# Performance work log

Measured on AMD Instinct MI355X. Metric: run time of the kernel, lower is better.

Reference implementation:

```python
import jax, jax.numpy as jnp
import numpy as np

# dims: d_model=96, d_expand=192, d_state N=16, dt_rank R=6, K=4 scans, 3x3 depthwise conv
B_, H_, W_, DM = 2, 64, 64, 96
DEXP, N, R, K, DCONV = 192, 16, 6, 4, 3


def setup_inputs() -> dict:
    key = jax.random.key(0)
    ks = jax.random.split(key, 8)
    s = lambda k, shape, scale: jax.random.normal(k, shape, jnp.float32) * scale
    return {
        "x": jax.random.normal(ks[0], (B_, H_, W_, DM), jnp.float32),
        "in_proj_w": s(ks[1], (2 * DEXP, DM), 0.05),          # Linear(d_model -> 2*d_expand), no bias
        "conv_w": s(ks[2], (DEXP, 1, DCONV, DCONV), 0.1),     # depthwise conv2d
        "conv_b": jnp.zeros((DEXP,), jnp.float32),
        "x_proj_weight": s(ks[3], (K, R + 2 * N, DEXP), 0.05),
        "dt_projs_weight": s(ks[4], (K, DEXP, R), 0.1),
        "dt_projs_bias": s(ks[5], (K, DEXP), 0.1),
        "A_logs": jnp.tile(jnp.log(jnp.arange(1, N + 1, dtype=jnp.float32))[None, :], (K * DEXP, 1)),
        "Ds": jnp.ones((K * DEXP,), jnp.float32),
        "out_norm_scale": jnp.ones((DEXP,), jnp.float32),
        "out_norm_bias": jnp.zeros((DEXP,), jnp.float32),
        "out_proj_w": s(ks[6], (DM, DEXP), 0.05),             # Linear(d_expand -> d_model), no bias
    }


def _selective_scan(u, delta, A, Bmat, Cmat, Ds):
    # u, delta: (B,K,D,L); A: (K,D,N); Bmat, Cmat: (B,K,N,L); Ds: (K,D)
    Bb, Kk, Dd, L = u.shape
    u_t = jnp.moveaxis(u, -1, 0)      # (L,B,K,D)
    d_t = jnp.moveaxis(delta, -1, 0)  # (L,B,K,D)
    B_t = jnp.moveaxis(Bmat, -1, 0)   # (L,B,K,N)
    C_t = jnp.moveaxis(Cmat, -1, 0)   # (L,B,K,N)
    h0 = jnp.zeros((Bb, Kk, Dd, A.shape[-1]), u.dtype)

    def step(h, inp):
        dt, ut, bt, ct = inp
        dA = jnp.exp(dt[..., None] * A)                      # (B,K,D,N)
        h = dA * h + (dt * ut)[..., None] * bt[:, :, None, :]
        y = jnp.einsum('bkdn,bkn->bkd', h, ct)
        return h, y

    _, ys = jax.lax.scan(step, h0, (d_t, u_t, B_t, C_t))
    ys = jnp.moveaxis(ys, 0, -1)                             # (B,K,D,L)
    return ys + u * Ds[None, :, :, None]


def reference(x, in_proj_w, conv_w, conv_b, x_proj_weight, dt_projs_weight,
              dt_projs_bias, A_logs, Ds, out_norm_scale, out_norm_bias, out_proj_w):
    B, H, W, _ = x.shape
    L = H * W
    # in_proj then split into ssm branch and gate
    xz = x @ in_proj_w.T                                     # (B,H,W,2*DEXP)
    xp, z = jnp.split(xz, 2, axis=-1)
    z = jax.nn.silu(z)
    # depthwise conv (NCHW) + SiLU
    xc = jnp.transpose(xp, (0, 3, 1, 2))                     # (B,DEXP,H,W)
    xc = jax.lax.conv_general_dilated(
        xc, conv_w, (1, 1), [(1, 1), (1, 1)],
        dimension_numbers=('NCHW', 'OIHW', 'NCHW'),
        feature_group_count=DEXP) + conv_b[None, :, None, None]
    xc = jax.nn.silu(xc)
    # multi-directional scan: h, h_flip, v, v_flip  (v = flatten in (w h) order)
    xh = xc.reshape(B, DEXP, L)
    xv = jnp.transpose(xc, (0, 1, 3, 2)).reshape(B, DEXP, L)
    xs = jnp.stack([xh, xh[..., ::-1], xv, xv[..., ::-1]], axis=1)  # (B,K,D,L)
    # per-direction projections
    x_dbl = jnp.einsum('bkdl,kcd->bkcl', xs, x_proj_weight)
    dts, Bs, Cs = jnp.split(x_dbl, [R, R + N], axis=2)
    dts = jnp.einsum('bkrl,kdr->bkdl', dts, dt_projs_weight)
    delta = jax.nn.softplus(dts + dt_projs_bias[None, :, :, None])
    A = -jnp.exp(A_logs).reshape(K, DEXP, N)
    ys = _selective_scan(xs, delta, A, Bs, Cs, Ds.reshape(K, DEXP))  # (B,K,D,L)
    # merge: reverse each scan back to row-major order, then sum
    yh = ys[:, 0]
    yhf = ys[:, 1][..., ::-1]
    yv = jnp.transpose(ys[:, 2].reshape(B, DEXP, W, H), (0, 1, 3, 2)).reshape(B, DEXP, L)
    yvf = jnp.transpose(ys[:, 3][..., ::-1].reshape(B, DEXP, W, H), (0, 1, 3, 2)).reshape(B, DEXP, L)
    y = jnp.transpose(yh + yhf + yv + yvf, (0, 2, 1))        # (B,L,DEXP)
    # out LayerNorm
    mu = y.mean(-1, keepdims=True)
    var = y.var(-1, keepdims=True)
    y = (y - mu) / jnp.sqrt(var + 1e-5) * out_norm_scale + out_norm_bias
    y = y.reshape(B, H, W, DEXP) * z                          # gate
    return y @ out_proj_w.T                                   # (B,H,W,DM)
```

## Files before the change

kernel.cpp:

```cpp
#include <hip/hip_runtime.h>
#include <math.h>

#define B_   2
#define H_   64
#define W_   64
#define DM   96
#define DE   192
#define NST  16
#define RNK  6
#define KD   4
#define L_   (H_*W_)
#define LQ   (B_*L_)
#define BK   (B_*KD)
#define NCHUNK 128
#define LC   (L_/NCHUNK)

#define SZ_PLANE  (DE*LQ)
#define OFF_YSH0  0
#define OFF_YSH1  (1*SZ_PLANE)
#define OFF_YSV0  (2*SZ_PLANE)
#define OFF_YSV1  (3*SZ_PLANE)
#define OFF_ZS    (4*SZ_PLANE)
#define OFF_XCHN  (5*SZ_PLANE)
#define OFF_XCVN  (6*SZ_PLANE)
#define OFF_DTC   (7*SZ_PLANE)
#define SZ_DTC    (BK*L_*8)
#define OFF_BC    (OFF_DTC + SZ_DTC)
#define SZ_BC     (BK*L_*32)
#define OFF_AP    (OFF_BC + SZ_BC)
#define SZ_SUMM   (BK*NCHUNK*DE*NST)
#define OFF_HL    (OFF_AP + SZ_SUMM)

__device__ __forceinline__ float silu(float x) { return x / (1.f + __expf(-x)); }
__device__ __forceinline__ int vtrans(int l) { return ((l & 63) << 6) | (l >> 6); }
__device__ __forceinline__ float softplus_f(float x) {
    return (x > 20.f) ? x : __logf(1.f + __expf(x));
}

__device__ __forceinline__ void pow16(float e1, float* a) {
    a[0] = e1;
    a[1] = a[0] * a[0];
    a[2] = a[1] * a[0];
    a[3] = a[1] * a[1];
    a[4] = a[3] * a[0];
    a[5] = a[3] * a[1];
    a[6] = a[3] * a[2];
    a[7] = a[3] * a[3];
    a[8] = a[7] * a[0];
    a[9] = a[7] * a[1];
    a[10] = a[7] * a[2];
    a[11] = a[7] * a[3];
    a[12] = a[7] * a[4];
    a[13] = a[7] * a[5];
    a[14] = a[7] * a[6];
    a[15] = a[7] * a[7];
}

#define TRW 64
#define XPAD 68
#define WPAD 104
__global__ void __launch_bounds__(192) k_inproj(
        const float* __restrict__ x, const float* __restrict__ Wp,
        float* __restrict__ xpT, float* __restrict__ zs) {
    __shared__ float xl[DM * XPAD];
    __shared__ float wl[DM * WPAD];
    int r0 = blockIdx.x * TRW;
    int o0 = blockIdx.y * DM;
    int t = threadIdx.x;

    for (int e = t; e < TRW * DM; e += 192) {
        int rr = e / DM, i = e % DM;
        xl[i * XPAD + rr] = x[(size_t)(r0 + rr) * DM + i];
    }
    for (int e = t; e < DM * DM; e += 192) {
        int c = e / DM, i = e % DM;
        wl[i * WPAD + c] = Wp[(size_t)(o0 + c) * DM + i];
    }
    __syncthreads();

    int rg = t & 15, cg = t >> 4;
    float acc[4][8];
#pragma unroll
    for (int r = 0; r < 4; ++r)
#pragma unroll
        for (int c = 0; c < 8; ++c) acc[r][c] = 0.f;

#pragma unroll 4
    for (int i = 0; i < DM; ++i) {
        float4 x4 = *(const float4*)&xl[i * XPAD + rg * 4];
        float4 wa = *(const float4*)&wl[i * WPAD + cg * 8];
        float4 wb = *(const float4*)&wl[i * WPAD + cg * 8 + 4];
        const float* xv = &x4.x;
        const float* wv0 = &wa.x;
        const float* wv1 = &wb.x;
#pragma unroll
        for (int r = 0; r < 4; ++r) {
#pragma unroll
            for (int c = 0; c < 4; ++c) {
                acc[r][c] = fmaf(xv[r], wv0[c], acc[r][c]);
                acc[r][c + 4] = fmaf(xv[r], wv1[c], acc[r][c + 4]);
            }
        }
    }

    if (o0 < DE) {
        __syncthreads();
        float* ol = wl;
#pragma unroll
        for (int r = 0; r < 4; ++r)
#pragma unroll
            for (int c = 0; c < 8; ++c)
                ol[(cg * 8 + c) * 65 + rg * 4 + r] = acc[r][c];
        __syncthreads();
        for (int e = t; e < DM * TRW; e += 192) {
            int c = e >> 6, r = e & 63;
            xpT[(size_t)(o0 + c) * LQ + r0 + r] = ol[c * 65 + r];
        }
    } else {
        int zc = o0 - DE + cg * 8;
#pragma unroll
        for (int r = 0; r < 4; ++r) {
            int row = r0 + rg * 4 + r;
            float4 za = make_float4(silu(acc[r][0]), silu(acc[r][1]), silu(acc[r][2]), silu(acc[r][3]));
            float4 zb = make_float4(silu(acc[r][4]), silu(acc[r][5]), silu(acc[r][6]), silu(acc[r][7]));
            *(float4*)&zs[(size_t)row * DE + zc] = za;
            *(float4*)&zs[(size_t)row * DE + zc + 4] = zb;
        }
    }
}

__global__ void __launch_bounds__(256) k_conv(
        const float* __restrict__ xpT, const float* __restrict__ cw,
        const float* __restrict__ cb, float* __restrict__ xch, float* __restrict__ xcv) {
    __shared__ float sv[4][65];
    int d = blockIdx.y, b = blockIdx.z;
    int wq = threadIdx.x & 63, hh = threadIdx.x >> 6;
    int h = blockIdx.x * 4 + hh;
    const float* src = xpT + (size_t)d * LQ + b * L_;
    float acc = cb[d];
#pragma unroll
    for (int dy = -1; dy <= 1; ++dy) {
        int hy = h + dy;
        if (hy < 0 || hy >= H_) continue;
#pragma unroll
        for (int dx = -1; dx <= 1; ++dx) {
            int wx = wq + dx;
            if (wx < 0 || wx >= W_) continue;
            acc += src[hy * W_ + wx] * cw[d * 9 + (dy + 1) * 3 + (dx + 1)];
        }
    }
    float val = silu(acc);
    xch[(size_t)d * LQ + b * L_ + h * W_ + wq] = val;
    sv[hh][wq] = val;
    __syncthreads();
    int w2 = threadIdx.x >> 2, hh2 = threadIdx.x & 3;
    xcv[(size_t)d * LQ + b * L_ + w2 * H_ + blockIdx.x * 4 + hh2] = sv[hh2][w2];
}

__global__ void __launch_bounds__(256) k_transp(
        const float* __restrict__ xch, const float* __restrict__ xcv,
        float* __restrict__ xchn, float* __restrict__ xcvn) {
    __shared__ float s[64][65];
    const float* src = blockIdx.z ? xcv : xch;
    float* dst = blockIdx.z ? xcvn : xchn;
    int r0 = blockIdx.x * 64, d0 = blockIdx.y * 64;
    int t = threadIdx.x;
#pragma unroll
    for (int i = 0; i < 16; ++i) {
        int idx = i * 256 + t;
        int dd = idx >> 6, ll = idx & 63;
        s[dd][ll] = src[(size_t)(d0 + dd) * LQ + r0 + ll];
    }
    __syncthreads();
#pragma unroll
    for (int i = 0; i < 16; ++i) {
        int idx = i * 256 + t;
        int ll = idx >> 6, dd = idx & 63;
        dst[(size_t)(r0 + ll) * DE + d0 + dd] = s[dd][ll];
    }
}

__global__ void __launch_bounds__(256) k_xdbl(
        const float* __restrict__ xch, const float* __restrict__ xcv,
        const float* __restrict__ xpw, float* __restrict__ dtc, float* __restrict__ bcv) {
    __shared__ float wl[DE * 40];
    int k = blockIdx.y, b = blockIdx.z;
    int t = threadIdx.x;
    for (int idx = t; idx < 38 * DE; idx += 256) {
        int c = idx / DE, d = idx % DE;
        wl[d * 40 + c] = xpw[(size_t)k * 38 * DE + idx];
    }
    __syncthreads();
    int l = blockIdx.x * 256 + t;
    int lp = (k & 1) ? (L_ - 1 - l) : l;
    const float* src = ((k < 2) ? xch : xcv) + b * L_ + lp;
    float acc[38];
#pragma unroll
    for (int c = 0; c < 38; ++c) acc[c] = 0.f;
#pragma unroll 2
    for (int d = 0; d < DE; ++d) {
        float v = src[(size_t)d * LQ];
        const float4* wr = (const float4*)&wl[d * 40];
#pragma unroll
        for (int q = 0; q < 9; ++q) {
            float4 w4 = wr[q];
            acc[q * 4 + 0] += v * w4.x;
            acc[q * 4 + 1] += v * w4.y;
            if (q * 4 + 2 < 38) acc[q * 4 + 2] += v * w4.z;
            if (q * 4 + 3 < 38) acc[q * 4 + 3] += v * w4.w;
        }
        acc[36] += v * wl[d * 40 + 36];
        acc[37] += v * wl[d * 40 + 37];
    }
    int bk = b * KD + k;
    float* dst = dtc + ((size_t)bk * L_ + l) * 8;
    *(float4*)dst = make_float4(acc[0], acc[1], acc[2], acc[3]);
    *(float4*)(dst + 4) = make_float4(acc[4], acc[5], 0.f, 0.f);
    float* row = bcv + ((size_t)bk * L_ + l) * 32;
#pragma unroll
    for (int j = 0; j < 8; ++j)
        *(float4*)(row + j * 4) = make_float4(acc[RNK + j * 4], acc[RNK + j * 4 + 1],
                                              acc[RNK + j * 4 + 2], acc[RNK + j * 4 + 3]);
}

__global__ void __launch_bounds__(192) k_scanA(
        const float* __restrict__ dtc, const float* __restrict__ dtw,
        const float* __restrict__ dtb, const float* __restrict__ xchn,
        const float* __restrict__ xcvn, const float* __restrict__ bc,
        float* __restrict__ ap_, float* __restrict__ hl_) {
    int chunk = blockIdx.x, k = blockIdx.y, b = blockIdx.z;
    int d = threadIdx.x;
    int bk = b * KD + k;
    int rev = k & 1;
    float w6[RNK];
#pragma unroll
    for (int r = 0; r < RNK; ++r) w6[r] = dtw[((size_t)k * DE + d) * RNK + r];
    float bias = dtb[k * DE + d];
    const float* uarr = ((k < 2) ? xchn : xcvn) + (size_t)b * L_ * DE;
    const float* dtrow = dtc + (size_t)bk * L_ * 8;
    const float* bcrow = bc + (size_t)bk * L_ * 32;
    int l0 = chunk * LC;
    float h[16];
#pragma unroll
    for (int n = 0; n < 16; ++n) h[n] = 0.f;
    float sdt = 0.f;

    int lp0 = rev ? (L_ - 1 - l0) : l0;
    float4 dA = *(const float4*)(dtrow + (size_t)l0 * 8);
    float2 dB = *(const float2*)(dtrow + (size_t)l0 * 8 + 4);
    float uu = uarr[(size_t)lp0 * DE + d];
    float4 Bq0 = *(const float4*)(bcrow + (size_t)l0 * 32);
    float4 Bq1 = *(const float4*)(bcrow + (size_t)l0 * 32 + 4);
    float4 Bq2 = *(const float4*)(bcrow + (size_t)l0 * 32 + 8);
    float4 Bq3 = *(const float4*)(bcrow + (size_t)l0 * 32 + 12);

    for (int ll = 0; ll < LC; ++ll) {
        float4 dA_c = dA; float2 dB_c = dB;
        float uu_c = uu;
        float4 B0 = Bq0, B1 = Bq1, B2 = Bq2, B3 = Bq3;
        if (ll + 1 < LC) {
            int l2 = l0 + ll + 1;
            int lp2 = rev ? (L_ - 1 - l2) : l2;
            dA = *(const float4*)(dtrow + (size_t)l2 * 8);
            dB = *(const float2*)(dtrow + (size_t)l2 * 8 + 4);
            uu = uarr[(size_t)lp2 * DE + d];
            Bq0 = *(const float4*)(bcrow + (size_t)l2 * 32);
            Bq1 = *(const float4*)(bcrow + (size_t)l2 * 32 + 4);
            Bq2 = *(const float4*)(bcrow + (size_t)l2 * 32 + 8);
            Bq3 = *(const float4*)(bcrow + (size_t)l2 * 32 + 12);
        }
        float dacc = bias + dA_c.x * w6[0] + dA_c.y * w6[1] + dA_c.z * w6[2]
                   + dA_c.w * w6[3] + dB_c.x * w6[4] + dB_c.y * w6[5];
        float dt = softplus_f(dacc);
        sdt += dt;
        float du = dt * uu_c;
        float a[16];
        pow16(__expf(-dt), a);
        float Bv[16];
        Bv[0]=B0.x; Bv[1]=B0.y; Bv[2]=B0.z; Bv[3]=B0.w;
        Bv[4]=B1.x; Bv[5]=B1.y; Bv[6]=B1.z; Bv[7]=B1.w;
        Bv[8]=B2.x; Bv[9]=B2.y; Bv[10]=B2.z; Bv[11]=B2.w;
        Bv[12]=B3.x; Bv[13]=B3.y; Bv[14]=B3.z; Bv[15]=B3.w;
#pragma unroll
        for (int n = 0; n < 16; ++n) h[n] = fmaf(a[n], h[n], du * Bv[n]);
    }
    float ap[16];
    pow16(__expf(-sdt), ap);
    size_t o = ((size_t)(bk * NCHUNK + chunk) * DE + d) * NST;
#pragma unroll
    for (int q = 0; q < 4; ++q) {
        *(float4*)(ap_ + o + q * 4) = make_float4(ap[q*4], ap[q*4+1], ap[q*4+2], ap[q*4+3]);
        *(float4*)(hl_ + o + q * 4) = make_float4(h[q*4], h[q*4+1], h[q*4+2], h[q*4+3]);
    }
}

__global__ void __launch_bounds__(256) k_scanB(
        const float* __restrict__ ap_, float* __restrict__ hl_) {
    int q = blockIdx.x * 256 + threadIdx.x;
    int bk = q / (DE * NST);
    int qq = q % (DE * NST);
    size_t base = (size_t)bk * NCHUNK * DE * NST + qq;
    const size_t stride = DE * NST;
    float carry = 0.f;
    float a = ap_[base], hv = hl_[base];
    for (int c = 0; c < NCHUNK; ++c) {
        size_t idx = base + (size_t)c * stride;
        float a_c = a, h_c = hv;
        if (c + 1 < NCHUNK) { a = ap_[idx + stride]; hv = hl_[idx + stride]; }
        hl_[idx] = carry;
        carry = fmaf(a_c, carry, h_c);
    }
}

__global__ void __launch_bounds__(192) k_scanC(
        const float* __restrict__ dtc, const float* __restrict__ dtw,
        const float* __restrict__ dtb, const float* __restrict__ xchn,
        const float* __restrict__ xcvn, const float* __restrict__ bc,
        const float* __restrict__ Ds, const float* __restrict__ hin,
        float* __restrict__ ysH0, float* __restrict__ ysH1,
        float* __restrict__ ysV0, float* __restrict__ ysV1) {
    int chunk = blockIdx.x, k = blockIdx.y, b = blockIdx.z;
    int d = threadIdx.x;
    int bk = b * KD + k;
    int rev = k & 1;
    float w6[RNK];
#pragma unroll
    for (int r = 0; r < RNK; ++r) w6[r] = dtw[((size_t)k * DE + d) * RNK + r];
    float bias = dtb[k * DE + d];
    float Dsk = Ds[k * DE + d];
    const float* uarr = ((k < 2) ? xchn : xcvn) + (size_t)b * L_ * DE;
    float* ysel = (k == 0) ? ysH0 : (k == 1) ? ysH1 : (k == 2) ? ysV0 : ysV1;
    float* ys = ysel + (size_t)b * L_ * DE;
    const float* dtrow = dtc + (size_t)bk * L_ * 8;
    const float* bcrow = bc + (size_t)bk * L_ * 32;
    int l0 = chunk * LC;
    float h[16];
    size_t o = ((size_t)(bk * NCHUNK + chunk) * DE + d) * NST;
#pragma unroll
    for (int q = 0; q < 4; ++q) {
        float4 h4 = *(const float4*)(hin + o + q * 4);
        h[q*4] = h4.x; h[q*4+1] = h4.y; h[q*4+2] = h4.z; h[q*4+3] = h4.w;
    }

    int lp0 = rev ? (L_ - 1 - l0) : l0;
    float4 dA = *(const float4*)(dtrow + (size_t)l0 * 8);
    float2 dB = *(const float2*)(dtrow + (size_t)l0 * 8 + 4);
    float uu = uarr[(size_t)lp0 * DE + d];
    float4 Bq0 = *(const float4*)(bcrow + (size_t)l0 * 32);
    float4 Bq1 = *(const float4*)(bcrow + (size_t)l0 * 32 + 4);
    float4 Bq2 = *(const float4*)(bcrow + (size_t)l0 * 32 + 8);
    float4 Bq3 = *(const float4*)(bcrow + (size_t)l0 * 32 + 12);
    float4 Cq0 = *(const float4*)(bcrow + (size_t)l0 * 32 + 16);
    float4 Cq1 = *(const float4*)(bcrow + (size_t)l0 * 32 + 20);
    float4 Cq2 = *(const float4*)(bcrow + (size_t)l0 * 32 + 24);
    float4 Cq3 = *(const float4*)(bcrow + (size_t)l0 * 32 + 28);

    for (int ll = 0; ll < LC; ++ll) {
        int l = l0 + ll;
        int lp = rev ? (L_ - 1 - l) : l;
        float4 dA_c = dA; float2 dB_c = dB;
        float uu_c = uu;
        float4 B0 = Bq0, B1 = Bq1, B2 = Bq2, B3 = Bq3;
        float4 C0 = Cq0, C1 = Cq1, C2 = Cq2, C3 = Cq3;
        if (ll + 1 < LC) {
            int l2 = l + 1;
            int lp2 = rev ? (L_ - 1 - l2) : l2;
            dA = *(const float4*)(dtrow + (size_t)l2 * 8);
            dB = *(const float2*)(dtrow + (size_t)l2 * 8 + 4);
            uu = uarr[(size_t)lp2 * DE + d];
            Bq0 = *(const float4*)(bcrow + (size_t)l2 * 32);
            Bq1 = *(const float4*)(bcrow + (size_t)l2 * 32 + 4);
            Bq2 = *(const float4*)(bcrow + (size_t)l2 * 32 + 8);
            Bq3 = *(const float4*)(bcrow + (size_t)l2 * 32 + 12);
            Cq0 = *(const float4*)(bcrow + (size_t)l2 * 32 + 16);
            Cq1 = *(const float4*)(bcrow + (size_t)l2 * 32 + 20);
            Cq2 = *(const float4*)(bcrow + (size_t)l2 * 32 + 24);
            Cq3 = *(const float4*)(bcrow + (size_t)l2 * 32 + 28);
        }
        float dacc = bias + dA_c.x * w6[0] + dA_c.y * w6[1] + dA_c.z * w6[2]
                   + dA_c.w * w6[3] + dB_c.x * w6[4] + dB_c.y * w6[5];
        float dt = softplus_f(dacc);
        float du = dt * uu_c;
        float a[16];
        pow16(__expf(-dt), a);
        float Bv[16], Cv[16];
        Bv[0]=B0.x; Bv[1]=B0.y; Bv[2]=B0.z; Bv[3]=B0.w;
        Bv[4]=B1.x; Bv[5]=B1.y; Bv[6]=B1.z; Bv[7]=B1.w;
        Bv[8]=B2.x; Bv[9]=B2.y; Bv[10]=B2.z; Bv[11]=B2.w;
        Bv[12]=B3.x; Bv[13]=B3.y; Bv[14]=B3.z; Bv[15]=B3.w;
        Cv[0]=C0.x; Cv[1]=C0.y; Cv[2]=C0.z; Cv[3]=C0.w;
        Cv[4]=C1.x; Cv[5]=C1.y; Cv[6]=C1.z; Cv[7]=C1.w;
        Cv[8]=C2.x; Cv[9]=C2.y; Cv[10]=C2.z; Cv[11]=C2.w;
        Cv[12]=C3.x; Cv[13]=C3.y; Cv[14]=C3.z; Cv[15]=C3.w;
        float p0 = 0.f, p1 = 0.f, p2 = 0.f, p3 = 0.f;
#pragma unroll
        for (int n = 0; n < 4; ++n) {
            h[n] = fmaf(a[n], h[n], du * Bv[n]);           p0 = fmaf(h[n], Cv[n], p0);
            h[n+4] = fmaf(a[n+4], h[n+4], du * Bv[n+4]);   p1 = fmaf(h[n+4], Cv[n+4], p1);
            h[n+8] = fmaf(a[n+8], h[n+8], du * Bv[n+8]);   p2 = fmaf(h[n+8], Cv[n+8], p2);
            h[n+12] = fmaf(a[n+12], h[n+12], du * Bv[n+12]); p3 = fmaf(h[n+12], Cv[n+12], p3);
        }
        float p = (p0 + p1) + (p2 + p3);
        ys[(size_t)lp * DE + d] = p + uu_c * Dsk;
    }
}

__global__ void __launch_bounds__(192) k_final(
        const float* __restrict__ ysH0, const float* __restrict__ ysH1,
        const float* __restrict__ ysV0, const float* __restrict__ ysV1,
        const float* __restrict__ lnw, const float* __restrict__ lnb,
        const float* __restrict__ zs, const float* __restrict__ Wout,
        float* __restrict__ out) {
    __shared__ float yrow[DE];
    __shared__ float pp[DE];
    __shared__ float red[2][3];
    int t = threadIdx.x;
    int o = t % DM, half = t / DM;
    float4 wreg[24];
    const float4* wrow = (const float4*)(Wout + (size_t)o * DE + half * 96);
#pragma unroll
    for (int q = 0; q < 24; ++q) wreg[q] = wrow[q];
    float lw = lnw[t], lb = lnb[t];
    int r0 = blockIdx.x * 16;
    for (int rr = 0; rr < 16; ++rr) {
        int r = r0 + rr;
        int b = r >> 12, l = r & (L_ - 1);
        int lv = vtrans(l);
        size_t base = (size_t)r * DE + t;
        size_t vbase = ((size_t)(b * L_) + lv) * DE + t;
        float s = ysH0[base] + ysH1[base] + ysV0[vbase] + ysV1[vbase];
        float sum = s, sq = s * s;
#pragma unroll
        for (int off = 32; off >= 1; off >>= 1) {
            sum += __shfl_xor(sum, off);
            sq  += __shfl_xor(sq, off);
        }
        if ((t & 63) == 0) { red[0][t >> 6] = sum; red[1][t >> 6] = sq; }
        __syncthreads();
        float tot = red[0][0] + red[0][1] + red[0][2];
        float totq = red[1][0] + red[1][1] + red[1][2];
        float mu = tot / DE;
        float var = totq / DE - mu * mu;
        float rstd = rsqrtf(var + 1e-5f);
        float yz = ((s - mu) * rstd * lw + lb) * zs[base];
        yrow[t] = yz;
        __syncthreads();
        float acc = 0.f;
        const float4* yr = (const float4*)&yrow[half * 96];
#pragma unroll
        for (int q = 0; q < 24; ++q) {
            float4 w4 = wreg[q], y4 = yr[q];
            acc += w4.x * y4.x + w4.y * y4.y + w4.z * y4.z + w4.w * y4.w;
        }
        pp[t] = acc;
        __syncthreads();
        if (t < DM) out[(size_t)r * DM + t] = pp[t] + pp[t + DM];
        __syncthreads();
    }
}

extern "C" void kernel_launch(void* const* d_in, const int* in_sizes, int n_in,
                              void* d_out, int out_size, void* d_ws, size_t ws_size,
                              hipStream_t stream) {
    const float* x    = (const float*)d_in[0];
    const float* Wp   = (const float*)d_in[1];
    const float* cw   = (const float*)d_in[2];
    const float* cb   = (const float*)d_in[3];
    const float* xpw  = (const float*)d_in[4];
    const float* dtw  = (const float*)d_in[5];
    const float* dtb  = (const float*)d_in[6];
    const float* Ds   = (const float*)d_in[8];
    const float* lnw  = (const float*)d_in[9];
    const float* lnb  = (const float*)d_in[10];
    const float* Wout = (const float*)d_in[11];
    float* out = (float*)d_out;

    float* ws = (float*)d_ws;
    float* ysH0  = ws + OFF_YSH0;
    float* ysH1  = ws + OFF_YSH1;
    float* ysV0  = ws + OFF_YSV0;
    float* ysV1  = ws + OFF_YSV1;
    float* xpT   = ws + OFF_YSH0;
    float* xch   = ws + OFF_YSH1;
    float* xcv   = ws + OFF_YSV0;
    float* zs    = ws + OFF_ZS;
    float* xchn  = ws + OFF_XCHN;
    float* xcvn  = ws + OFF_XCVN;
    float* dtc   = ws + OFF_DTC;
    float* bc    = ws + OFF_BC;
    float* ap    = ws + OFF_AP;
    float* hl    = ws + OFF_HL;

    k_inproj<<<dim3(LQ / TRW, 4), 192, 0, stream>>>(x, Wp, xpT, zs);
    k_conv<<<dim3(16, DE, B_), 256, 0, stream>>>(xpT, cw, cb, xch, xcv);
    k_transp<<<dim3(LQ / 64, DE / 64, 2), 256, 0, stream>>>(xch, xcv, xchn, xcvn);
    k_xdbl<<<dim3(L_ / 256, KD, B_), 256, 0, stream>>>(xch, xcv, xpw, dtc, bc);
    k_scanA<<<dim3(NCHUNK, KD, B_), 192, 0, stream>>>(dtc, dtw, dtb, xchn, xcvn, bc, ap, hl);
    k_scanB<<<(BK * DE * NST) / 256, 256, 0, stream>>>(ap, hl);
    k_scanC<<<dim3(NCHUNK, KD, B_), 192, 0, stream>>>(dtc, dtw, dtb, xchn, xcvn, bc, Ds, hl,
                                                      ysH0, ysH1, ysV0, ysV1);
    k_final<<<LQ / 16, 192, 0, stream>>>(ysH0, ysH1, ysV0, ysV1, lnw, lnb, zs, Wout, out);
}
```

Measured before the change: 262.1 us.

## Split x_proj across channel groups, merge dt/B/C rows, retune chunk and final sizes

The x_proj kernel is split across four channel groups of ten outputs each via an extra grid dimension. This cuts accumulator registers from 38 to 10 per thread and quadruples the block count, at the cost of re-reading the input once per group. The dt, B and C outputs are packed into a single 48-float row per position, which the two scan kernels now read. Separately, the scan chunk count drops from 128 to 64 (fewer, longer chunks and smaller summaries) and the final kernel processes 8 rows per block instead of 16.

```diff
diff --git a/kernel.cpp b/kernel.cpp
--- a/kernel.cpp
+++ b/kernel.cpp
@@ -12,7 +12,7 @@
 #define L_   (H_*W_)
 #define LQ   (B_*L_)
 #define BK   (B_*KD)
-#define NCHUNK 128
+#define NCHUNK 64
 #define LC   (L_/NCHUNK)
 
 #define SZ_PLANE  (DE*LQ)
@@ -23,13 +23,9 @@
 #define OFF_ZS    (4*SZ_PLANE)
 #define OFF_XCHN  (5*SZ_PLANE)
 #define OFF_XCVN  (6*SZ_PLANE)
-#define OFF_DTC   (7*SZ_PLANE)
-#define SZ_DTC    (BK*L_*8)
-#define OFF_BC    (OFF_DTC + SZ_DTC)
-#define SZ_BC     (BK*L_*32)
-#define OFF_AP    (OFF_BC + SZ_BC)
-#define SZ_SUMM   (BK*NCHUNK*DE*NST)
-#define OFF_HL    (OFF_AP + SZ_SUMM)
+#define OFF_ROWS  (7*SZ_PLANE)
+#define OFF_AP    (8*SZ_PLANE)
+#define OFF_HL    (9*SZ_PLANE)
 
 __device__ __forceinline__ float silu(float x) { return x / (1.f + __expf(-x)); }
 __device__ __forceinline__ int vtrans(int l) { return ((l & 63) << 6) | (l >> 6); }
@@ -182,52 +178,50 @@
 
 __global__ void __launch_bounds__(256) k_xdbl(
         const float* __restrict__ xch, const float* __restrict__ xcv,
-        const float* __restrict__ xpw, float* __restrict__ dtc, float* __restrict__ bcv) {
-    __shared__ float wl[DE * 40];
-    int k = blockIdx.y, b = blockIdx.z;
+        const float* __restrict__ xpw, float* __restrict__ rows) {
+    __shared__ float wl[DE * 12];
+    int cq = blockIdx.y;
+    int k = blockIdx.z & 3, b = blockIdx.z >> 2;
     int t = threadIdx.x;
-    for (int idx = t; idx < 38 * DE; idx += 256) {
-        int c = idx / DE, d = idx % DE;
-        wl[d * 40 + c] = xpw[(size_t)k * 38 * DE + idx];
+    for (int e = t; e < DE * 12; e += 256) {
+        int d = e / 12, j = e % 12;
+        int c = cq * 10 + j;
+        wl[e] = (j < 10 && c < 38) ? xpw[((size_t)k * 38 + c) * DE + d] : 0.f;
     }
     __syncthreads();
     int l = blockIdx.x * 256 + t;
     int lp = (k & 1) ? (L_ - 1 - l) : l;
     const float* src = ((k < 2) ? xch : xcv) + b * L_ + lp;
-    float acc[38];
-#pragma unroll
-    for (int c = 0; c < 38; ++c) acc[c] = 0.f;
-#pragma unroll 2
+    float a0 = 0, a1 = 0, a2 = 0, a3 = 0, a4 = 0, a5 = 0, a6 = 0, a7 = 0, a8 = 0, a9 = 0;
+#pragma unroll 4
     for (int d = 0; d < DE; ++d) {
         float v = src[(size_t)d * LQ];
-        const float4* wr = (const float4*)&wl[d * 40];
-#pragma unroll
-        for (int q = 0; q < 9; ++q) {
-            float4 w4 = wr[q];
-            acc[q * 4 + 0] += v * w4.x;
-            acc[q * 4 + 1] += v * w4.y;
-            if (q * 4 + 2 < 38) acc[q * 4 + 2] += v * w4.z;
-            if (q * 4 + 3 < 38) acc[q * 4 + 3] += v * w4.w;
-        }
-        acc[36] += v * wl[d * 40 + 36];
-        acc[37] += v * wl[d * 40 + 37];
+        float4 w0 = *(const float4*)&wl[d * 12];
+        float4 w1 = *(const float4*)&wl[d * 12 + 4];
+        float4 w2 = *(const float4*)&wl[d * 12 + 8];
+        a0 = fmaf(v, w0.x, a0); a1 = fmaf(v, w0.y, a1);
+        a2 = fmaf(v, w0.z, a2); a3 = fmaf(v, w0.w, a3);
+        a4 = fmaf(v, w1.x, a4); a5 = fmaf(v, w1.y, a5);
+        a6 = fmaf(v, w1.z, a6); a7 = fmaf(v, w1.w, a7);
+        a8 = fmaf(v, w2.x, a8); a9 = fmaf(v, w2.y, a9);
     }
     int bk = b * KD + k;
-    float* dst = dtc + ((size_t)bk * L_ + l) * 8;
-    *(float4*)dst = make_float4(acc[0], acc[1], acc[2], acc[3]);
-    *(float4*)(dst + 4) = make_float4(acc[4], acc[5], 0.f, 0.f);
-    float* row = bcv + ((size_t)bk * L_ + l) * 32;
-#pragma unroll
-    for (int j = 0; j < 8; ++j)
-        *(float4*)(row + j * 4) = make_float4(acc[RNK + j * 4], acc[RNK + j * 4 + 1],
-                                              acc[RNK + j * 4 + 2], acc[RNK + j * 4 + 3]);
+    float* row = rows + ((size_t)bk * L_ + l) * 48;
+    float acc[10] = {a0, a1, a2, a3, a4, a5, a6, a7, a8, a9};
+#pragma unroll
+    for (int j = 0; j < 10; ++j) {
+        int gc = cq * 10 + j;
+        if (gc < 38) {
+            int slot = (gc < 6) ? gc : (gc < 22) ? (8 + gc - 6) : (24 + gc - 22);
+            row[slot] = acc[j];
+        }
+    }
 }
 
 __global__ void __launch_bounds__(192) k_scanA(
-        const float* __restrict__ dtc, const float* __restrict__ dtw,
+        const float* __restrict__ rows, const float* __restrict__ dtw,
         const float* __restrict__ dtb, const float* __restrict__ xchn,
-        const float* __restrict__ xcvn, const float* __restrict__ bc,
-        float* __restrict__ ap_, float* __restrict__ hl_) {
+        const float* __restrict__ xcvn, float* __restrict__ ap_, float* __restrict__ hl_) {
     int chunk = blockIdx.x, k = blockIdx.y, b = blockIdx.z;
     int d = threadIdx.x;
     int bk = b * KD + k;
@@ -237,8 +231,7 @@
     for (int r = 0; r < RNK; ++r) w6[r] = dtw[((size_t)k * DE + d) * RNK + r];
     float bias = dtb[k * DE + d];
     const float* uarr = ((k < 2) ? xchn : xcvn) + (size_t)b * L_ * DE;
-    const float* dtrow = dtc + (size_t)bk * L_ * 8;
-    const float* bcrow = bc + (size_t)bk * L_ * 32;
+    const float* rw = rows + (size_t)bk * L_ * 48;
     int l0 = chunk * LC;
     float h[16];
 #pragma unroll
@@ -246,13 +239,13 @@
     float sdt = 0.f;
 
     int lp0 = rev ? (L_ - 1 - l0) : l0;
-    float4 dA = *(const float4*)(dtrow + (size_t)l0 * 8);
-    float2 dB = *(const float2*)(dtrow + (size_t)l0 * 8 + 4);
+    float4 dA = *(const float4*)(rw + (size_t)l0 * 48);
+    float2 dB = *(const float2*)(rw + (size_t)l0 * 48 + 4);
     float uu = uarr[(size_t)lp0 * DE + d];
-    float4 Bq0 = *(const float4*)(bcrow + (size_t)l0 * 32);
-    float4 Bq1 = *(const float4*)(bcrow + (size_t)l0 * 32 + 4);
-    float4 Bq2 = *(const float4*)(bcrow + (size_t)l0 * 32 + 8);
-    float4 Bq3 = *(const float4*)(bcrow + (size_t)l0 * 32 + 12);
+    float4 Bq0 = *(const float4*)(rw + (size_t)l0 * 48 + 8);
+    float4 Bq1 = *(const float4*)(rw + (size_t)l0 * 48 + 12);
+    float4 Bq2 = *(const float4*)(rw + (size_t)l0 * 48 + 16);
+    float4 Bq3 = *(const float4*)(rw + (size_t)l0 * 48 + 20);
 
     for (int ll = 0; ll < LC; ++ll) {
         float4 dA_c = dA; float2 dB_c = dB;
@@ -261,13 +254,13 @@
         if (ll + 1 < LC) {
             int l2 = l0 + ll + 1;
             int lp2 = rev ? (L_ - 1 - l2) : l2;
-            dA = *(const float4*)(dtrow + (size_t)l2 * 8);
-            dB = *(const float2*)(dtrow + (size_t)l2 * 8 + 4);
+            dA = *(const float4*)(rw + (size_t)l2 * 48);
+            dB = *(const float2*)(rw + (size_t)l2 * 48 + 4);
             uu = uarr[(size_t)lp2 * DE + d];
-            Bq0 = *(const float4*)(bcrow + (size_t)l2 * 32);
-            Bq1 = *(const float4*)(bcrow + (size_t)l2 * 32 + 4);
-            Bq2 = *(const float4*)(bcrow + (size_t)l2 * 32 + 8);
-            Bq3 = *(const float4*)(bcrow + (size_t)l2 * 32 + 12);
+            Bq0 = *(const float4*)(rw + (size_t)l2 * 48 + 8);
+            Bq1 = *(const float4*)(rw + (size_t)l2 * 48 + 12);
+            Bq2 = *(const float4*)(rw + (size_t)l2 * 48 + 16);
+            Bq3 = *(const float4*)(rw + (size_t)l2 * 48 + 20);
         }
         float dacc = bias + dA_c.x * w6[0] + dA_c.y * w6[1] + dA_c.z * w6[2]
                    + dA_c.w * w6[3] + dB_c.x * w6[4] + dB_c.y * w6[5];
@@ -313,10 +306,10 @@
 }
 
 __global__ void __launch_bounds__(192) k_scanC(
-        const float* __restrict__ dtc, const float* __restrict__ dtw,
+        const float* __restrict__ rows, const float* __restrict__ dtw,
         const float* __restrict__ dtb, const float* __restrict__ xchn,
-        const float* __restrict__ xcvn, const float* __restrict__ bc,
-        const float* __restrict__ Ds, const float* __restrict__ hin,
+        const float* __restrict__ xcvn, const float* __restrict__ Ds,
+        const float* __restrict__ hin,
         float* __restrict__ ysH0, float* __restrict__ ysH1,
         float* __restrict__ ysV0, float* __restrict__ ysV1) {
     int chunk = blockIdx.x, k = blockIdx.y, b = blockIdx.z;
@@ -331,8 +324,7 @@
     const float* uarr = ((k < 2) ? xchn : xcvn) + (size_t)b * L_ * DE;
     float* ysel = (k == 0) ? ysH0 : (k == 1) ? ysH1 : (k == 2) ? ysV0 : ysV1;
     float* ys = ysel + (size_t)b * L_ * DE;
-    const float* dtrow = dtc + (size_t)bk * L_ * 8;
-    const float* bcrow = bc + (size_t)bk * L_ * 32;
+    const float* rw = rows + (size_t)bk * L_ * 48;
     int l0 = chunk * LC;
     float h[16];
     size_t o = ((size_t)(bk * NCHUNK + chunk) * DE + d) * NST;
@@ -343,17 +335,17 @@
     }
 
     int lp0 = rev ? (L_ - 1 - l0) : l0;
-    float4 dA = *(const float4*)(dtrow + (size_t)l0 * 8);
-    float2 dB = *(const float2*)(dtrow + (size_t)l0 * 8 + 4);
+    float4 dA = *(const float4*)(rw + (size_t)l0 * 48);
+    float2 dB = *(const float2*)(rw + (size_t)l0 * 48 + 4);
     float uu = uarr[(size_t)lp0 * DE + d];
-    float4 Bq0 = *(const float4*)(bcrow + (size_t)l0 * 32);
-    float4 Bq1 = *(const float4*)(bcrow + (size_t)l0 * 32 + 4);
-    float4 Bq2 = *(const float4*)(bcrow + (size_t)l0 * 32 + 8);
-    float4 Bq3 = *(const float4*)(bcrow + (size_t)l0 * 32 + 12);
-    float4 Cq0 = *(const float4*)(bcrow + (size_t)l0 * 32 + 16);
-    float4 Cq1 = *(const float4*)(bcrow + (size_t)l0 * 32 + 20);
-    float4 Cq2 = *(const float4*)(bcrow + (size_t)l0 * 32 + 24);
-    float4 Cq3 = *(const float4*)(bcrow + (size_t)l0 * 32 + 28);
+    float4 Bq0 = *(const float4*)(rw + (size_t)l0 * 48 + 8);
+    float4 Bq1 = *(const float4*)(rw + (size_t)l0 * 48 + 12);
+    float4 Bq2 = *(const float4*)(rw + (size_t)l0 * 48 + 16);
+    float4 Bq3 = *(const float4*)(rw + (size_t)l0 * 48 + 20);
+    float4 Cq0 = *(const float4*)(rw + (size_t)l0 * 48 + 24);
+    float4 Cq1 = *(const float4*)(rw + (size_t)l0 * 48 + 28);
+    float4 Cq2 = *(const float4*)(rw + (size_t)l0 * 48 + 32);
+    float4 Cq3 = *(const float4*)(rw + (size_t)l0 * 48 + 36);
 
     for (int ll = 0; ll < LC; ++ll) {
         int l = l0 + ll;
@@ -365,17 +357,17 @@
         if (ll + 1 < LC) {
             int l2 = l + 1;
             int lp2 = rev ? (L_ - 1 - l2) : l2;
-            dA = *(const float4*)(dtrow + (size_t)l2 * 8);
-            dB = *(const float2*)(dtrow + (size_t)l2 * 8 + 4);
+            dA = *(const float4*)(rw + (size_t)l2 * 48);
+            dB = *(const float2*)(rw + (size_t)l2 * 48 + 4);
             uu = uarr[(size_t)lp2 * DE + d];
-            Bq0 = *(const float4*)(bcrow + (size_t)l2 * 32);
-            Bq1 = *(const float4*)(bcrow + (size_t)l2 * 32 + 4);
-            Bq2 = *(const float4*)(bcrow + (size_t)l2 * 32 + 8);
-            Bq3 = *(const float4*)(bcrow + (size_t)l2 * 32 + 12);
-            Cq0 = *(const float4*)(bcrow + (size_t)l2 * 32 + 16);
-            Cq1 = *(const float4*)(bcrow + (size_t)l2 * 32 + 20);
-            Cq2 = *(const float4*)(bcrow + (size_t)l2 * 32 + 24);
-            Cq3 = *(const float4*)(bcrow + (size_t)l2 * 32 + 28);
+            Bq0 = *(const float4*)(rw + (size_t)l2 * 48 + 8);
+            Bq1 = *(const float4*)(rw + (size_t)l2 * 48 + 12);
+            Bq2 = *(const float4*)(rw + (size_t)l2 * 48 + 16);
+            Bq3 = *(const float4*)(rw + (size_t)l2 * 48 + 20);
+            Cq0 = *(const float4*)(rw + (size_t)l2 * 48 + 24);
+            Cq1 = *(const float4*)(rw + (size_t)l2 * 48 + 28);
+            Cq2 = *(const float4*)(rw + (size_t)l2 * 48 + 32);
+            Cq3 = *(const float4*)(rw + (size_t)l2 * 48 + 36);
         }
         float dacc = bias + dA_c.x * w6[0] + dA_c.y * w6[1] + dA_c.z * w6[2]
                    + dA_c.w * w6[3] + dB_c.x * w6[4] + dB_c.y * w6[5];
@@ -395,9 +387,9 @@
         float p0 = 0.f, p1 = 0.f, p2 = 0.f, p3 = 0.f;
 #pragma unroll
         for (int n = 0; n < 4; ++n) {
-            h[n] = fmaf(a[n], h[n], du * Bv[n]);           p0 = fmaf(h[n], Cv[n], p0);
-            h[n+4] = fmaf(a[n+4], h[n+4], du * Bv[n+4]);   p1 = fmaf(h[n+4], Cv[n+4], p1);
-            h[n+8] = fmaf(a[n+8], h[n+8], du * Bv[n+8]);   p2 = fmaf(h[n+8], Cv[n+8], p2);
+            h[n] = fmaf(a[n], h[n], du * Bv[n]);             p0 = fmaf(h[n], Cv[n], p0);
+            h[n+4] = fmaf(a[n+4], h[n+4], du * Bv[n+4]);     p1 = fmaf(h[n+4], Cv[n+4], p1);
+            h[n+8] = fmaf(a[n+8], h[n+8], du * Bv[n+8]);     p2 = fmaf(h[n+8], Cv[n+8], p2);
             h[n+12] = fmaf(a[n+12], h[n+12], du * Bv[n+12]); p3 = fmaf(h[n+12], Cv[n+12], p3);
         }
         float p = (p0 + p1) + (p2 + p3);
@@ -421,8 +413,8 @@
 #pragma unroll
     for (int q = 0; q < 24; ++q) wreg[q] = wrow[q];
     float lw = lnw[t], lb = lnb[t];
-    int r0 = blockIdx.x * 16;
-    for (int rr = 0; rr < 16; ++rr) {
+    int r0 = blockIdx.x * 8;
+    for (int rr = 0; rr < 8; ++rr) {
         int r = r0 + rr;
         int b = r >> 12, l = r & (L_ - 1);
         int lv = vtrans(l);
@@ -486,18 +478,17 @@
     float* zs    = ws + OFF_ZS;
     float* xchn  = ws + OFF_XCHN;
     float* xcvn  = ws + OFF_XCVN;
-    float* dtc   = ws + OFF_DTC;
-    float* bc    = ws + OFF_BC;
+    float* rows  = ws + OFF_ROWS;
     float* ap    = ws + OFF_AP;
     float* hl    = ws + OFF_HL;
 
     k_inproj<<<dim3(LQ / TRW, 4), 192, 0, stream>>>(x, Wp, xpT, zs);
     k_conv<<<dim3(16, DE, B_), 256, 0, stream>>>(xpT, cw, cb, xch, xcv);
     k_transp<<<dim3(LQ / 64, DE / 64, 2), 256, 0, stream>>>(xch, xcv, xchn, xcvn);
-    k_xdbl<<<dim3(L_ / 256, KD, B_), 256, 0, stream>>>(xch, xcv, xpw, dtc, bc);
-    k_scanA<<<dim3(NCHUNK, KD, B_), 192, 0, stream>>>(dtc, dtw, dtb, xchn, xcvn, bc, ap, hl);
+    k_xdbl<<<dim3(L_ / 256, 4, KD * B_), 256, 0, stream>>>(xch, xcv, xpw, rows);
+    k_scanA<<<dim3(NCHUNK, KD, B_), 192, 0, stream>>>(rows, dtw, dtb, xchn, xcvn, ap, hl);
     k_scanB<<<(BK * DE * NST) / 256, 256, 0, stream>>>(ap, hl);
-    k_scanC<<<dim3(NCHUNK, KD, B_), 192, 0, stream>>>(dtc, dtw, dtb, xchn, xcvn, bc, Ds, hl,
+    k_scanC<<<dim3(NCHUNK, KD, B_), 192, 0, stream>>>(rows, dtw, dtb, xchn, xcvn, Ds, hl,
                                                       ysH0, ysH1, ysV0, ysV1);
-    k_final<<<LQ / 16, 192, 0, stream>>>(ysH0, ysH1, ysV0, ysV1, lnw, lnb, zs, Wout, out);
-}
+    k_final<<<LQ / 8, 192, 0, stream>>>(ysH0, ysH1, ysV0, ysV1, lnw, lnb, zs, Wout, out);
+}
```

Result: faster. 248.0 us (-5.4%).
